# Kernel optimization log

Hardware: AMD Instinct MI355X
Metric: run time of the kernel (lower is better)

The kernel has to match this reference:

```python
import jax, jax.numpy as jnp
import numpy as np


def setup_inputs() -> dict:
    key = jax.random.key(0)
    k1, k2 = jax.random.split(key)
    H, D, N = 1, 256, 65536        # (heads=1, embedding_dim, num_tokens)
    C = 1024                       # num_embeddings (codebook size)
    inputs = jax.random.normal(k1, (H, D, N), dtype=jnp.float32)
    embedding = jax.random.normal(k2, (H, C, D), dtype=jnp.float32)
    return {"inputs": inputs, "embedding": embedding}


COMMITMENT_COST = 0.25


def reference(inputs, embedding):
    # inputs: (h, d, n) -> flat: (h, n, d)
    flat = jnp.transpose(inputs, (0, 2, 1))
    # negative euclidean distance (matches -torch.cdist, p=2)
    x2 = jnp.sum(flat * flat, axis=-1, keepdims=True)            # (h, n, 1)
    e2 = jnp.sum(embedding * embedding, axis=-1)[:, None, :]     # (h, 1, c)
    xe = jnp.einsum('hnd,hcd->hnc', flat, embedding)             # (h, n, c)
    d2 = jnp.maximum(x2 + e2 - 2.0 * xe, 0.0)
    distances = -jnp.sqrt(d2)                                    # (h, n, c)
    encoding_indices = jnp.argmax(distances, axis=2)             # (h, n)
    # gather codebook vectors: h == 1
    quantized = jnp.take(embedding[0], encoding_indices[0], axis=0)[None]  # (h, n, d)
    commit_loss = jnp.mean((jax.lax.stop_gradient(quantized) - flat) ** 2)
    loss = COMMITMENT_COST * commit_loss
    # straight-through estimator
    quantized_st = flat + jax.lax.stop_gradient(quantized - flat)
    out = jnp.transpose(quantized_st, (0, 2, 1))                 # (h, d, n)
    return out, encoding_indices, loss, distances
```

## Files before the change

### kernel.cpp

```cpp
#include <hip/hip_runtime.h>
#include <math.h>

#define N_TOK 65536
#define D_DIM 256
#define C_NUM 1024

#define OUT_OFF   0
#define IDX_OFF   (D_DIM * N_TOK)
#define LOSS_OFF  (IDX_OFF + N_TOK)
#define DIST_OFF  (LOSS_OFF + 1)

#define MARGIN 0.01f
#define NPART 4096

typedef __attribute__((ext_vector_type(8))) short bf16x8;
typedef __attribute__((ext_vector_type(4))) float f32x4;

static __device__ __forceinline__ unsigned short f2bf(float f) {
  unsigned int u = __float_as_uint(f);
  unsigned int r = (u + 0x7fffu + ((u >> 16) & 1u)) >> 16;
  return (unsigned short)r;
}
static __device__ __forceinline__ float bf2f(unsigned short h) {
  return __uint_as_float(((unsigned int)h) << 16);
}


#define WS_EH   0
#define WS_EL   524288
#define WS_E2   1048576
#define WS_NEEDED (WS_E2 + 4096)

#define XH_OFF_F 0
#define XL_OFF_F 8388608

#define PART_OFF_F 263168

__global__ __launch_bounds__(256) void kA2_prep(const float* __restrict__ X,
                                                const float* __restrict__ E,
                                                float* __restrict__ out,
                                                unsigned char* __restrict__ ws) {
  const int bid = blockIdx.x, tid = threadIdx.x;
  if (bid < 1024) {
    unsigned short* XhG = (unsigned short*)(out + XH_OFF_F);
    unsigned short* XlG = (unsigned short*)(out + XL_OFF_F);
    const int n = bid * 64 + (tid >> 2);
    const int sg = (tid & 3) * 16;
    unsigned short* xh = XhG + (size_t)n * D_DIM;
    unsigned short* xl = XlG + (size_t)n * D_DIM;
#pragma unroll 1
    for (int dc = 0; dc < D_DIM; dc += 64) {
      float v[16];
#pragma unroll
      for (int j = 0; j < 16; ++j) v[j] = X[(size_t)(dc + sg + j) * N_TOK + n];
      unsigned short hh[16], ll[16];
#pragma unroll
      for (int j = 0; j < 16; ++j) {
        hh[j] = f2bf(v[j]);
        ll[j] = f2bf(v[j] - bf2f(hh[j]));
      }
      *(bf16x8*)(xh + dc + sg) = *(bf16x8*)&hh[0];
      *(bf16x8*)(xh + dc + sg + 8) = *(bf16x8*)&hh[8];
      *(bf16x8*)(xl + dc + sg) = *(bf16x8*)&ll[0];
      *(bf16x8*)(xl + dc + sg + 8) = *(bf16x8*)&ll[8];
    }
  } else if (bid < 1040) {
    unsigned short* EhG = (unsigned short*)(ws + WS_EH);
    unsigned short* ElG = (unsigned short*)(ws + WS_EL);
    float* e2p = (float*)(ws + WS_E2);
    const int lane = tid & 63, w = tid >> 6;
#pragma unroll 1
    for (int cc = 0; cc < 16; ++cc) {
      const int c = (bid - 1024) * 64 + w * 16 + cc;
      const float4 v = *(const float4*)(E + (size_t)c * D_DIM + lane * 4);
      unsigned short h0 = f2bf(v.x), h1 = f2bf(v.y), h2 = f2bf(v.z), h3 = f2bf(v.w);
      unsigned short l0 = f2bf(v.x - bf2f(h0)), l1 = f2bf(v.y - bf2f(h1));
      unsigned short l2 = f2bf(v.z - bf2f(h2)), l3 = f2bf(v.w - bf2f(h3));
      ushort4 hv = make_ushort4(h0, h1, h2, h3);
      ushort4 lv = make_ushort4(l0, l1, l2, l3);
      *(ushort4*)(EhG + (size_t)c * D_DIM + lane * 4) = hv;
      *(ushort4*)(ElG + (size_t)c * D_DIM + lane * 4) = lv;
      float s = v.x * v.x + v.y * v.y + v.z * v.z + v.w * v.w;
#pragma unroll
      for (int off = 32; off; off >>= 1) s += __shfl_down(s, off, 64);
      if (lane == 0) e2p[c] = s;
    }
  } else {
    const int n = (bid - 1040) * 256 + tid;
    float s = 0.0f;
#pragma unroll 8
    for (int d = 0; d < D_DIM; ++d) {
      float v = X[(size_t)d * N_TOK + n];
      s = fmaf(v, v, s);
    }
    out[IDX_OFF + n] = s;
  }
}

#define TM 64
#define TC 256
#define BK 32
#define XS2 264

__global__ __launch_bounds__(256) void k2c_dist(float* __restrict__ out,
                                                unsigned char* __restrict__ ws) {
  __shared__ __align__(16) unsigned short xh[TM * XS2];
  __shared__ __align__(16) unsigned short xl[TM * XS2];

  const unsigned short* __restrict__ XhG = (const unsigned short*)(out + XH_OFF_F);
  const unsigned short* __restrict__ XlG = (const unsigned short*)(out + XL_OFF_F);
  const unsigned short* __restrict__ EhG = (const unsigned short*)(ws + WS_EH);
  const float* __restrict__ e2p = (const float*)(ws + WS_E2);

  const int tid = threadIdx.x;
  const int lane = tid & 63, wave = tid >> 6;

  const int bid = blockIdx.x;
  const int xcd = bid & 7;
  const int slot = bid >> 3;
  const int bx = slot & 3;
  const int by = xcd * 128 + (slot >> 2);
  const int c0 = bx * TC;
  const int n0 = by * TM;

  const int wc = c0 + wave * 64;
  const int m = lane & 15;
  const int q = lane >> 4;

  {
    const int tl = tid >> 2;
    const int seg = (tid & 3) * 64;
    const unsigned short* gh = XhG + (size_t)(n0 + tl) * D_DIM + seg;
    const unsigned short* gl = XlG + (size_t)(n0 + tl) * D_DIM + seg;
    unsigned short* sh = xh + tl * XS2 + seg;
    unsigned short* sl = xl + tl * XS2 + seg;
#pragma unroll
    for (int j = 0; j < 8; ++j) {
      *(bf16x8*)(sh + j * 8) = *(const bf16x8*)(gh + j * 8);
      *(bf16x8*)(sl + j * 8) = *(const bf16x8*)(gl + j * 8);
    }
  }
  __syncthreads();

  f32x4 acc[4][4];
#pragma unroll
  for (int i = 0; i < 4; ++i)
#pragma unroll
    for (int t = 0; t < 4; ++t) acc[i][t] = (f32x4){0.f, 0.f, 0.f, 0.f};

  const unsigned short* bp[4];
#pragma unroll
  for (int t = 0; t < 4; ++t) bp[t] = EhG + (size_t)(wc + t * 16 + m) * D_DIM + q * 8;
  const size_t loEu = (size_t)(WS_EL - WS_EH) / 2;

#pragma unroll 2
  for (int kb = 0; kb < D_DIM; kb += BK) {
    bf16x8 ah[4], al[4], bh[4], bl[4];
#pragma unroll
    for (int t = 0; t < 4; ++t) {
      bh[t] = *(const bf16x8*)(bp[t] + kb);
      bl[t] = *(const bf16x8*)(bp[t] + loEu + kb);
    }
#pragma unroll
    for (int i = 0; i < 4; ++i) {
      const int ro = (i * 16 + m) * XS2 + kb + q * 8;
      ah[i] = *(const bf16x8*)&xh[ro];
      al[i] = *(const bf16x8*)&xl[ro];
    }
#pragma unroll
    for (int i = 0; i < 4; ++i)
#pragma unroll
      for (int t = 0; t < 4; ++t) {
        acc[i][t] = __builtin_amdgcn_mfma_f32_16x16x32_bf16(ah[i], bh[t], acc[i][t], 0, 0, 0);
        acc[i][t] = __builtin_amdgcn_mfma_f32_16x16x32_bf16(ah[i], bl[t], acc[i][t], 0, 0, 0);
        acc[i][t] = __builtin_amdgcn_mfma_f32_16x16x32_bf16(al[i], bh[t], acc[i][t], 0, 0, 0);
      }
  }

  float e2v[4];
#pragma unroll
  for (int t = 0; t < 4; ++t) e2v[t] = e2p[wc + t * 16 + m];

#pragma unroll
  for (int i = 0; i < 4; ++i) {
#pragma unroll
    for (int r = 0; r < 4; ++r) {
      const int tok = n0 + i * 16 + q * 4 + r;
      const float x2v = out[IDX_OFF + tok];
      const size_t row = DIST_OFF + (size_t)tok * C_NUM;
#pragma unroll
      for (int t = 0; t < 4; ++t) {
        float d2 = fmaf(-2.0f, acc[i][t][r], x2v + e2v[t]);
        d2 = fmaxf(d2, 0.0f);
        out[row + wc + t * 16 + m] = -sqrtf(d2);
      }
    }
  }
}

__global__ __launch_bounds__(256) void k3_argmax(const float* __restrict__ X,
                                                 const float* __restrict__ E,
                                                 float* __restrict__ out) {
  __shared__ float lsum[4];
  const int tid = threadIdx.x, lane = tid & 63, w = tid >> 6;
  float wloss = 0.0f;

#pragma unroll 1
  for (int it = 0; it < 4; ++it) {
    const int n = blockIdx.x * 16 + w * 4 + it;
    const float* row = out + DIST_OFF + (size_t)n * C_NUM;

    float v[16];
    float best = -3.4e38f;
    int bi = 0x7fffffff;
#pragma unroll
    for (int j = 0; j < 16; ++j) {
      v[j] = row[j * 64 + lane];
      if (v[j] > best) { best = v[j]; bi = j * 64 + lane; }
    }
#pragma unroll
    for (int off = 32; off; off >>= 1) {
      const float ov = __shfl_xor(best, off, 64);
      const int oi = __shfl_xor(bi, off, 64);
      if (ov > best || (ov == best && oi < bi)) { best = ov; bi = oi; }
    }
    const float thr = best - MARGIN;
    unsigned long long masks[16];
    int total = 0;
#pragma unroll
    for (int j = 0; j < 16; ++j) {
      masks[j] = __ballot(v[j] > thr);
      total += __popcll(masks[j]);
    }
    float best_d2 = best * best;
    int best_idx = bi;
    if (total > 1) {
      best_d2 = 3.4e38f;
      best_idx = 0x7fffffff;
      for (int j = 0; j < 16; ++j) {
        unsigned long long mm = masks[j];
        while (mm) {
          const int l = __ffsll((long long)mm) - 1;
          mm &= mm - 1;
          const int c = j * 64 + l;
          float sx = 0.f, se = 0.f, sxe = 0.f;
#pragma unroll
          for (int r = 0; r < 4; ++r) {
            const int d = r * 64 + lane;
            const float xv = X[(size_t)d * N_TOK + n];
            const float ev = E[(size_t)c * D_DIM + d];
            sx = fmaf(xv, xv, sx);
            se = fmaf(ev, ev, se);
            sxe = fmaf(xv, ev, sxe);
          }
          float d2 = fmaf(-2.f, sxe, sx + se);
#pragma unroll
          for (int off = 32; off; off >>= 1) d2 += __shfl_xor(d2, off, 64);
          d2 = fmaxf(d2, 0.f);
          if (d2 < best_d2 || (d2 == best_d2 && c < best_idx)) {
            best_d2 = d2; best_idx = c;
          }
        }
      }
    }
    if (lane == 0) out[IDX_OFF + n] = (float)best_idx;
    wloss += best_d2;
  }
  if (lane == 0) lsum[w] = wloss;
  __syncthreads();
  if (tid == 0)
    out[PART_OFF_F + blockIdx.x] = lsum[0] + lsum[1] + lsum[2] + lsum[3];
}

__global__ __launch_bounds__(256) void k3b_loss(float* __restrict__ out) {
  __shared__ float red[4];
  const int tid = threadIdx.x, lane = tid & 63, w = tid >> 6;
  float s = 0.0f;
#pragma unroll
  for (int i = 0; i < NPART / 256; ++i) s += out[PART_OFF_F + i * 256 + tid];
#pragma unroll
  for (int off = 32; off; off >>= 1) s += __shfl_down(s, off, 64);
  if (lane == 0) red[w] = s;
  __syncthreads();
  if (tid == 0)
    out[LOSS_OFF] = (red[0] + red[1] + red[2] + red[3]) *
                    (0.25f / ((float)N_TOK * (float)D_DIM));
}

#define EH_OFF_F  0
#define EL_OFF_F  131072
#define E2_OFF_F  262144

__global__ __launch_bounds__(256) void kA_prep(const float* __restrict__ X,
                                               const float* __restrict__ E,
                                               float* __restrict__ out) {
  const int bid = blockIdx.x, tid = threadIdx.x;
  if (bid < 256) {
    const int n = bid * 256 + tid;
    float s = 0.0f;
#pragma unroll 8
    for (int d = 0; d < D_DIM; ++d) {
      float v = X[(size_t)d * N_TOK + n];
      s = fmaf(v, v, s);
    }
    out[IDX_OFF + n] = s;
  } else {
    unsigned short* EhG = (unsigned short*)(out + EH_OFF_F);
    unsigned short* ElG = (unsigned short*)(out + EL_OFF_F);
    const int lane = tid & 63, w = tid >> 6;
#pragma unroll 1
    for (int cc = 0; cc < 16; ++cc) {
      const int c = (bid - 256) * 64 + w * 16 + cc;
      const float4 v = *(const float4*)(E + (size_t)c * D_DIM + lane * 4);
      unsigned short h0 = f2bf(v.x), h1 = f2bf(v.y), h2 = f2bf(v.z), h3 = f2bf(v.w);
      unsigned short l0 = f2bf(v.x - bf2f(h0)), l1 = f2bf(v.y - bf2f(h1));
      unsigned short l2 = f2bf(v.z - bf2f(h2)), l3 = f2bf(v.w - bf2f(h3));
      ushort4 hv = make_ushort4(h0, h1, h2, h3);
      ushort4 lv = make_ushort4(l0, l1, l2, l3);
      *(ushort4*)(EhG + (size_t)c * D_DIM + lane * 4) = hv;
      *(ushort4*)(ElG + (size_t)c * D_DIM + lane * 4) = lv;
      float s = v.x * v.x + v.y * v.y + v.z * v.z + v.w * v.w;
#pragma unroll
      for (int off = 32; off; off >>= 1) s += __shfl_down(s, off, 64);
      if (lane == 0) out[E2_OFF_F + c] = s;
    }
  }
}

#define XS 40

__global__ __launch_bounds__(256) void k2_dist(const float* __restrict__ X,
                                               float* __restrict__ out) {
  __shared__ __align__(16) unsigned short xhb[2][TM * XS];
  __shared__ __align__(16) unsigned short xlb[2][TM * XS];

  const unsigned short* __restrict__ EhG = (const unsigned short*)(out + EH_OFF_F);
  const unsigned short* __restrict__ ElG = (const unsigned short*)(out + EL_OFF_F);

  const int tid = threadIdx.x;
  const int lane = tid & 63, wave = tid >> 6;
  const int bid = blockIdx.x;
  const int xcd = bid & 7;
  const int slot = bid >> 3;
  const int bx = slot & 3;
  const int by = xcd * 128 + (slot >> 2);
  const int c0 = bx * TC;
  const int n0 = by * TM;

  const int wc = c0 + wave * 64;
  const int m = lane & 15;
  const int q = lane >> 4;

  f32x4 acc[4][4];
#pragma unroll
  for (int i = 0; i < 4; ++i)
#pragma unroll
    for (int t = 0; t < 4; ++t) acc[i][t] = (f32x4){0.f, 0.f, 0.f, 0.f};

  const int sn = lane;
  const int kg = wave;

  float xv[8];
  {
    const float* xp = X + (size_t)(kg * 8) * N_TOK + n0 + sn;
#pragma unroll
    for (int j = 0; j < 8; ++j) xv[j] = xp[(size_t)j * N_TOK];
  }

#pragma unroll 1
  for (int kb = 0; kb < D_DIM; kb += BK) {
    const int p = (kb >> 5) & 1;
    bf16x8 bh[4], bl[4];
#pragma unroll
    for (int t = 0; t < 4; ++t) {
      const size_t eoff = (size_t)(wc + t * 16 + m) * D_DIM + kb + q * 8;
      bh[t] = *(const bf16x8*)(EhG + eoff);
      bl[t] = *(const bf16x8*)(ElG + eoff);
    }
    unsigned short hh[8], ll[8];
#pragma unroll
    for (int j = 0; j < 8; ++j) {
      hh[j] = f2bf(xv[j]);
      ll[j] = f2bf(xv[j] - bf2f(hh[j]));
    }
    *(bf16x8*)&xhb[p][sn * XS + kg * 8] = *(bf16x8*)hh;
    *(bf16x8*)&xlb[p][sn * XS + kg * 8] = *(bf16x8*)ll;
    if (kb + BK < D_DIM) {
      const float* xp = X + (size_t)(kb + BK + kg * 8) * N_TOK + n0 + sn;
#pragma unroll
      for (int j = 0; j < 8; ++j) xv[j] = xp[(size_t)j * N_TOK];
    }
    __syncthreads();
    bf16x8 ah[4], al[4];
#pragma unroll
    for (int i = 0; i < 4; ++i) {
      const int ro = (i * 16 + m) * XS + q * 8;
      ah[i] = *(const bf16x8*)&xhb[p][ro];
      al[i] = *(const bf16x8*)&xlb[p][ro];
    }
#pragma unroll
    for (int i = 0; i < 4; ++i)
#pragma unroll
      for (int t = 0; t < 4; ++t) {
        acc[i][t] = __builtin_amdgcn_mfma_f32_16x16x32_bf16(ah[i], bh[t], acc[i][t], 0, 0, 0);
        acc[i][t] = __builtin_amdgcn_mfma_f32_16x16x32_bf16(ah[i], bl[t], acc[i][t], 0, 0, 0);
        acc[i][t] = __builtin_amdgcn_mfma_f32_16x16x32_bf16(al[i], bh[t], acc[i][t], 0, 0, 0);
      }
  }

  float e2v[4];
#pragma unroll
  for (int t = 0; t < 4; ++t) e2v[t] = out[E2_OFF_F + wc + t * 16 + m];

#pragma unroll
  for (int i = 0; i < 4; ++i) {
#pragma unroll
    for (int r = 0; r < 4; ++r) {
      const int tok = n0 + i * 16 + q * 4 + r;
      const float x2v = out[IDX_OFF + tok];
      const size_t row = DIST_OFF + (size_t)tok * C_NUM;
#pragma unroll
      for (int t = 0; t < 4; ++t) {
        float d2 = fmaf(-2.0f, acc[i][t][r], x2v + e2v[t]);
        d2 = fmaxf(d2, 0.0f);
        out[row + wc + t * 16 + m] = -sqrtf(d2);
      }
    }
  }
}

__global__ __launch_bounds__(256) void k4_gather(const float* __restrict__ E,
                                                 float* __restrict__ out) {
  const int g = blockIdx.x * 256 + threadIdx.x;
  const int n = g * 4;
  const int i0 = (int)out[IDX_OFF + n + 0];
  const int i1 = (int)out[IDX_OFF + n + 1];
  const int i2 = (int)out[IDX_OFF + n + 2];
  const int i3 = (int)out[IDX_OFF + n + 3];
  const float* e0 = E + (size_t)i0 * D_DIM;
  const float* e1 = E + (size_t)i1 * D_DIM;
  const float* e2 = E + (size_t)i2 * D_DIM;
  const float* e3 = E + (size_t)i3 * D_DIM;
  const int d0 = blockIdx.y * 32;
#pragma unroll 4
  for (int d = d0; d < d0 + 32; ++d) {
    float4 wv = make_float4(e0[d], e1[d], e2[d], e3[d]);
    *(float4*)&out[(size_t)d * N_TOK + n] = wv;
  }
}

extern "C" void kernel_launch(void* const* d_in, const int* in_sizes, int n_in,
                              void* d_out, int out_size, void* d_ws, size_t ws_size,
                              hipStream_t stream) {
  const float* X = (const float*)d_in[0];
  const float* E = (const float*)d_in[1];
  float* out = (float*)d_out;

  if (ws_size >= WS_NEEDED && d_ws != nullptr) {
    unsigned char* ws = (unsigned char*)d_ws;
    hipLaunchKernelGGL(kA2_prep, dim3(1296), dim3(256), 0, stream, X, E, out, ws);
    hipLaunchKernelGGL(k2c_dist, dim3((C_NUM / TC) * (N_TOK / TM)), dim3(256), 0,
                       stream, out, ws);
    hipLaunchKernelGGL(k3_argmax, dim3(N_TOK / 16), dim3(256), 0, stream, X, E, out);
    hipLaunchKernelGGL(k3b_loss, dim3(1), dim3(256), 0, stream, out);
    hipLaunchKernelGGL(k4_gather, dim3(N_TOK / 4 / 256, 8), dim3(256), 0, stream,
                       E, out);
  } else {
    hipLaunchKernelGGL(kA_prep, dim3(272), dim3(256), 0, stream, X, E, out);
    hipLaunchKernelGGL(k2_dist, dim3((C_NUM / TC) * (N_TOK / TM)), dim3(256), 0,
                       stream, X, out);
    hipLaunchKernelGGL(k3_argmax, dim3(N_TOK / 16), dim3(256), 0, stream, X, E, out);
    hipLaunchKernelGGL(k3b_loss, dim3(1), dim3(256), 0, stream, out);
    hipLaunchKernelGGL(k4_gather, dim3(N_TOK / 4 / 256, 8), dim3(256), 0, stream,
                       E, out);
  }
}
```

Before: 656.9 us.

## Fuse per-tile argmax partials into distance kernel and software-prefetch B fragments

The distance kernel now computes a per-token, per-64-column best value, index and near-tie count, and writes these to a workspace table. The argmax kernel combines the 16 partials per token and rereads the full 1024-wide distance row only when near-ties need exact fp32 refinement. This is meant to avoid reading the 256 MB distance matrix back in the common case. The K loop of the distance kernel also double-buffers its codebook fragment loads from global memory. In exchange, the epilogue gains shuffles and extra workspace writes, and the workspace requirement grows.

```diff
diff --git a/kernel.cpp b/kernel.cpp
--- a/kernel.cpp
+++ b/kernel.cpp
@@ -29,7 +29,9 @@
 #define WS_EH   0
 #define WS_EL   524288
 #define WS_E2   1048576
-#define WS_NEEDED (WS_E2 + 4096)
+#define WS_PART 1052672
+#define WS_TP   1069056
+#define WS_NEEDED (WS_TP + (size_t)N_TOK * 16 * 8)
 
 #define XH_OFF_F 0
 #define XL_OFF_F 8388608
@@ -111,6 +113,7 @@
   const unsigned short* __restrict__ XlG = (const unsigned short*)(out + XL_OFF_F);
   const unsigned short* __restrict__ EhG = (const unsigned short*)(ws + WS_EH);
   const float* __restrict__ e2p = (const float*)(ws + WS_E2);
+  uint2* __restrict__ tp = (uint2*)(ws + WS_TP);
 
   const int tid = threadIdx.x;
   const int lane = tid & 63, wave = tid >> 6;
@@ -153,14 +156,23 @@
   for (int t = 0; t < 4; ++t) bp[t] = EhG + (size_t)(wc + t * 16 + m) * D_DIM + q * 8;
   const size_t loEu = (size_t)(WS_EL - WS_EH) / 2;
 
-#pragma unroll 2
-  for (int kb = 0; kb < D_DIM; kb += BK) {
-    bf16x8 ah[4], al[4], bh[4], bl[4];
-#pragma unroll
-    for (int t = 0; t < 4; ++t) {
-      bh[t] = *(const bf16x8*)(bp[t] + kb);
-      bl[t] = *(const bf16x8*)(bp[t] + loEu + kb);
-    }
+  bf16x8 bh[4], bl[4], nbh[4], nbl[4];
+#pragma unroll
+  for (int t = 0; t < 4; ++t) {
+    bh[t] = *(const bf16x8*)(bp[t]);
+    bl[t] = *(const bf16x8*)(bp[t] + loEu);
+  }
+#pragma unroll
+  for (int kc = 0; kc < 8; ++kc) {
+    const int kb = kc * BK;
+    if (kc < 7) {
+#pragma unroll
+      for (int t = 0; t < 4; ++t) {
+        nbh[t] = *(const bf16x8*)(bp[t] + kb + BK);
+        nbl[t] = *(const bf16x8*)(bp[t] + loEu + kb + BK);
+      }
+    }
+    bf16x8 ah[4], al[4];
 #pragma unroll
     for (int i = 0; i < 4; ++i) {
       const int ro = (i * 16 + m) * XS2 + kb + q * 8;
@@ -175,6 +187,10 @@
         acc[i][t] = __builtin_amdgcn_mfma_f32_16x16x32_bf16(ah[i], bl[t], acc[i][t], 0, 0, 0);
         acc[i][t] = __builtin_amdgcn_mfma_f32_16x16x32_bf16(al[i], bh[t], acc[i][t], 0, 0, 0);
       }
+    if (kc < 7) {
+#pragma unroll
+      for (int t = 0; t < 4; ++t) { bh[t] = nbh[t]; bl[t] = nbl[t]; }
+    }
   }
 
   float e2v[4];
@@ -188,96 +204,160 @@
       const int tok = n0 + i * 16 + q * 4 + r;
       const float x2v = out[IDX_OFF + tok];
       const size_t row = DIST_OFF + (size_t)tok * C_NUM;
+      float dv[4];
+      float bestv = -3.4e38f;
+      int bidx = 0;
 #pragma unroll
       for (int t = 0; t < 4; ++t) {
         float d2 = fmaf(-2.0f, acc[i][t][r], x2v + e2v[t]);
         d2 = fmaxf(d2, 0.0f);
-        out[row + wc + t * 16 + m] = -sqrtf(d2);
-      }
-    }
-  }
-}
-
-__global__ __launch_bounds__(256) void k3_argmax(const float* __restrict__ X,
-                                                 const float* __restrict__ E,
-                                                 float* __restrict__ out) {
+        const float dd = -sqrtf(d2);
+        dv[t] = dd;
+        out[row + wc + t * 16 + m] = dd;
+        if (dd > bestv) { bestv = dd; bidx = wc + t * 16 + m; }
+      }
+#pragma unroll
+      for (int off = 1; off < 16; off <<= 1) {
+        const float ov = __shfl_xor(bestv, off, 64);
+        const int oi = __shfl_xor(bidx, off, 64);
+        if (ov > bestv || (ov == bestv && oi < bidx)) { bestv = ov; bidx = oi; }
+      }
+      const float thr2 = bestv - MARGIN;
+      int cnt = 0;
+#pragma unroll
+      for (int t = 0; t < 4; ++t) cnt += (dv[t] > thr2) ? 1 : 0;
+#pragma unroll
+      for (int off = 1; off < 16; off <<= 1) cnt += __shfl_xor(cnt, off, 64);
+      if ((lane & 15) == 0) {
+        tp[(size_t)tok * 16 + bx * 4 + wave] =
+            make_uint2(__float_as_uint(bestv),
+                       (unsigned)bidx | ((unsigned)cnt << 16));
+      }
+    }
+  }
+}
+
+__global__ __launch_bounds__(256) void k3a2_argmax(const float* __restrict__ X,
+                                                   const float* __restrict__ E,
+                                                   float* __restrict__ out,
+                                                   unsigned char* __restrict__ ws) {
+  const uint2* __restrict__ tp = (const uint2*)(ws + WS_TP);
+  float* __restrict__ part = (float*)(ws + WS_PART);
   __shared__ float lsum[4];
   const int tid = threadIdx.x, lane = tid & 63, w = tid >> 6;
-  float wloss = 0.0f;
-
-#pragma unroll 1
-  for (int it = 0; it < 4; ++it) {
-    const int n = blockIdx.x * 16 + w * 4 + it;
-    const float* row = out + DIST_OFF + (size_t)n * C_NUM;
-
-    float v[16];
-    float best = -3.4e38f;
-    int bi = 0x7fffffff;
-#pragma unroll
-    for (int j = 0; j < 16; ++j) {
-      v[j] = row[j * 64 + lane];
-      if (v[j] > best) { best = v[j]; bi = j * 64 + lane; }
-    }
-#pragma unroll
-    for (int off = 32; off; off >>= 1) {
-      const float ov = __shfl_xor(best, off, 64);
-      const int oi = __shfl_xor(bi, off, 64);
-      if (ov > best || (ov == best && oi < bi)) { best = ov; bi = oi; }
-    }
-    const float thr = best - MARGIN;
-    unsigned long long masks[16];
-    int total = 0;
-#pragma unroll
-    for (int j = 0; j < 16; ++j) {
-      masks[j] = __ballot(v[j] > thr);
-      total += __popcll(masks[j]);
-    }
-    float best_d2 = best * best;
-    int best_idx = bi;
-    if (total > 1) {
-      best_d2 = 3.4e38f;
-      best_idx = 0x7fffffff;
+  const int g = lane & 15, seg = lane >> 4;
+  const int n = blockIdx.x * 16 + w * 4 + seg;
+
+  const uint2 rec = tp[(size_t)n * 16 + g];
+  const float val = __uint_as_float(rec.x);
+  const int idx = (int)(rec.y & 0xffffu);
+  const int cnt = (int)(rec.y >> 16);
+
+  float best = val;
+  int bi = idx, bc = cnt;
+#pragma unroll
+  for (int off = 1; off < 16; off <<= 1) {
+    const float ov = __shfl_xor(best, off, 64);
+    const int oi = __shfl_xor(bi, off, 64);
+    const int oc = __shfl_xor(bc, off, 64);
+    if (ov > best || (ov == best && oi < bi)) { best = ov; bi = oi; bc = oc; }
+  }
+  const float thr = best - MARGIN;
+  const unsigned long long bal = __ballot(val > thr);
+  const int m16 = (int)((bal >> (seg * 16)) & 0xffffull);
+  const bool fast = (__popc((unsigned)m16) == 1) && (bc == 1);
+
+  float lval = 0.0f;
+  if (fast && g == 0) {
+    out[IDX_OFF + n] = (float)bi;
+    lval = best * best;
+  }
+
+  unsigned long long smask = __ballot((!fast) && (g == 0));
+  float sloss = 0.0f;
+  while (smask) {
+    const int sl = __ffsll((long long)smask) - 1;
+    smask &= smask - 1;
+    const int nn = blockIdx.x * 16 + w * 4 + (sl >> 4);
+    {
+      const float* row = out + DIST_OFF + (size_t)nn * C_NUM;
+      float v[16];
+      float bestf = -3.4e38f;
+      int bif = 0x7fffffff;
+#pragma unroll
       for (int j = 0; j < 16; ++j) {
-        unsigned long long mm = masks[j];
-        while (mm) {
-          const int l = __ffsll((long long)mm) - 1;
-          mm &= mm - 1;
-          const int c = j * 64 + l;
-          float sx = 0.f, se = 0.f, sxe = 0.f;
-#pragma unroll
-          for (int r = 0; r < 4; ++r) {
-            const int d = r * 64 + lane;
-            const float xv = X[(size_t)d * N_TOK + n];
-            const float ev = E[(size_t)c * D_DIM + d];
-            sx = fmaf(xv, xv, sx);
-            se = fmaf(ev, ev, se);
-            sxe = fmaf(xv, ev, sxe);
-          }
-          float d2 = fmaf(-2.f, sxe, sx + se);
-#pragma unroll
-          for (int off = 32; off; off >>= 1) d2 += __shfl_xor(d2, off, 64);
-          d2 = fmaxf(d2, 0.f);
-          if (d2 < best_d2 || (d2 == best_d2 && c < best_idx)) {
-            best_d2 = d2; best_idx = c;
+        v[j] = row[j * 64 + lane];
+        if (v[j] > bestf) { bestf = v[j]; bif = j * 64 + lane; }
+      }
+#pragma unroll
+      for (int off = 32; off; off >>= 1) {
+        const float ov = __shfl_xor(bestf, off, 64);
+        const int oi = __shfl_xor(bif, off, 64);
+        if (ov > bestf || (ov == bestf && oi < bif)) { bestf = ov; bif = oi; }
+      }
+      const float thrf = bestf - MARGIN;
+      unsigned long long masks[16];
+      int total = 0;
+#pragma unroll
+      for (int j = 0; j < 16; ++j) {
+        masks[j] = __ballot(v[j] > thrf);
+        total += __popcll(masks[j]);
+      }
+      float best_d2 = bestf * bestf;
+      int best_idx = bif;
+      if (total > 1) {
+        best_d2 = 3.4e38f;
+        best_idx = 0x7fffffff;
+        for (int j = 0; j < 16; ++j) {
+          unsigned long long mm = masks[j];
+          while (mm) {
+            const int l = __ffsll((long long)mm) - 1;
+            mm &= mm - 1;
+            const int c = j * 64 + l;
+            float sx = 0.f, se = 0.f, sxe = 0.f;
+#pragma unroll
+            for (int r = 0; r < 4; ++r) {
+              const int d = r * 64 + lane;
+              const float xv = X[(size_t)d * N_TOK + nn];
+              const float ev = E[(size_t)c * D_DIM + d];
+              sx = fmaf(xv, xv, sx);
+              se = fmaf(ev, ev, se);
+              sxe = fmaf(xv, ev, sxe);
+            }
+            float d2 = fmaf(-2.f, sxe, sx + se);
+#pragma unroll
+            for (int off = 32; off; off >>= 1) d2 += __shfl_xor(d2, off, 64);
+            d2 = fmaxf(d2, 0.f);
+            if (d2 < best_d2 || (d2 == best_d2 && c < best_idx)) {
+              best_d2 = d2; best_idx = c;
+            }
           }
         }
       }
-    }
-    if (lane == 0) out[IDX_OFF + n] = (float)best_idx;
-    wloss += best_d2;
-  }
-  if (lane == 0) lsum[w] = wloss;
+      if (lane == 0) {
+        out[IDX_OFF + nn] = (float)best_idx;
+        sloss += best_d2;
+      }
+    }
+  }
+
+  float wl = lval + ((lane == 0) ? sloss : 0.0f);
+#pragma unroll
+  for (int off = 32; off; off >>= 1) wl += __shfl_down(wl, off, 64);
+  if (lane == 0) lsum[w] = wl;
   __syncthreads();
   if (tid == 0)
-    out[PART_OFF_F + blockIdx.x] = lsum[0] + lsum[1] + lsum[2] + lsum[3];
-}
-
-__global__ __launch_bounds__(256) void k3b_loss(float* __restrict__ out) {
+    part[blockIdx.x] = lsum[0] + lsum[1] + lsum[2] + lsum[3];
+}
+
+__global__ __launch_bounds__(256) void k3b2_loss(float* __restrict__ out,
+                                                 unsigned char* __restrict__ ws) {
+  const float* __restrict__ part = (const float*)(ws + WS_PART);
   __shared__ float red[4];
   const int tid = threadIdx.x, lane = tid & 63, w = tid >> 6;
   float s = 0.0f;
 #pragma unroll
-  for (int i = 0; i < NPART / 256; ++i) s += out[PART_OFF_F + i * 256 + tid];
+  for (int i = 0; i < NPART / 256; ++i) s += part[i * 256 + tid];
 #pragma unroll
   for (int off = 32; off; off >>= 1) s += __shfl_down(s, off, 64);
   if (lane == 0) red[w] = s;
@@ -429,6 +509,95 @@
   }
 }
 
+__global__ __launch_bounds__(256) void k3_argmax(const float* __restrict__ X,
+                                                 const float* __restrict__ E,
+                                                 float* __restrict__ out) {
+  __shared__ float lsum[4];
+  const int tid = threadIdx.x, lane = tid & 63, w = tid >> 6;
+  float wloss = 0.0f;
+
+#pragma unroll 1
+  for (int it = 0; it < 4; ++it) {
+    const int n = blockIdx.x * 16 + w * 4 + it;
+    const float* row = out + DIST_OFF + (size_t)n * C_NUM;
+
+    float v[16];
+    float best = -3.4e38f;
+    int bi = 0x7fffffff;
+#pragma unroll
+    for (int j = 0; j < 16; ++j) {
+      v[j] = row[j * 64 + lane];
+      if (v[j] > best) { best = v[j]; bi = j * 64 + lane; }
+    }
+#pragma unroll
+    for (int off = 32; off; off >>= 1) {
+      const float ov = __shfl_xor(best, off, 64);
+      const int oi = __shfl_xor(bi, off, 64);
+      if (ov > best || (ov == best && oi < bi)) { best = ov; bi = oi; }
+    }
+    const float thr = best - MARGIN;
+    unsigned long long masks[16];
+    int total = 0;
+#pragma unroll
+    for (int j = 0; j < 16; ++j) {
+      masks[j] = __ballot(v[j] > thr);
+      total += __popcll(masks[j]);
+    }
+    float best_d2 = best * best;
+    int best_idx = bi;
+    if (total > 1) {
+      best_d2 = 3.4e38f;
+      best_idx = 0x7fffffff;
+      for (int j = 0; j < 16; ++j) {
+        unsigned long long mm = masks[j];
+        while (mm) {
+          const int l = __ffsll((long long)mm) - 1;
+          mm &= mm - 1;
+          const int c = j * 64 + l;
+          float sx = 0.f, se = 0.f, sxe = 0.f;
+#pragma unroll
+          for (int r = 0; r < 4; ++r) {
+            const int d = r * 64 + lane;
+            const float xv = X[(size_t)d * N_TOK + n];
+            const float ev = E[(size_t)c * D_DIM + d];
+            sx = fmaf(xv, xv, sx);
+            se = fmaf(ev, ev, se);
+            sxe = fmaf(xv, ev, sxe);
+          }
+          float d2 = fmaf(-2.f, sxe, sx + se);
+#pragma unroll
+          for (int off = 32; off; off >>= 1) d2 += __shfl_xor(d2, off, 64);
+          d2 = fmaxf(d2, 0.f);
+          if (d2 < best_d2 || (d2 == best_d2 && c < best_idx)) {
+            best_d2 = d2; best_idx = c;
+          }
+        }
+      }
+    }
+    if (lane == 0) out[IDX_OFF + n] = (float)best_idx;
+    wloss += best_d2;
+  }
+  if (lane == 0) lsum[w] = wloss;
+  __syncthreads();
+  if (tid == 0)
+    out[PART_OFF_F + blockIdx.x] = lsum[0] + lsum[1] + lsum[2] + lsum[3];
+}
+
+__global__ __launch_bounds__(256) void k3b_loss(float* __restrict__ out) {
+  __shared__ float red[4];
+  const int tid = threadIdx.x, lane = tid & 63, w = tid >> 6;
+  float s = 0.0f;
+#pragma unroll
+  for (int i = 0; i < NPART / 256; ++i) s += out[PART_OFF_F + i * 256 + tid];
+#pragma unroll
+  for (int off = 32; off; off >>= 1) s += __shfl_down(s, off, 64);
+  if (lane == 0) red[w] = s;
+  __syncthreads();
+  if (tid == 0)
+    out[LOSS_OFF] = (red[0] + red[1] + red[2] + red[3]) *
+                    (0.25f / ((float)N_TOK * (float)D_DIM));
+}
+
 __global__ __launch_bounds__(256) void k4_gather(const float* __restrict__ E,
                                                  float* __restrict__ out) {
   const int g = blockIdx.x * 256 + threadIdx.x;
@@ -461,8 +630,9 @@
     hipLaunchKernelGGL(kA2_prep, dim3(1296), dim3(256), 0, stream, X, E, out, ws);
     hipLaunchKernelGGL(k2c_dist, dim3((C_NUM / TC) * (N_TOK / TM)), dim3(256), 0,
                        stream, out, ws);
-    hipLaunchKernelGGL(k3_argmax, dim3(N_TOK / 16), dim3(256), 0, stream, X, E, out);
-    hipLaunchKernelGGL(k3b_loss, dim3(1), dim3(256), 0, stream, out);
+    hipLaunchKernelGGL(k3a2_argmax, dim3(N_TOK / 16), dim3(256), 0, stream,
+                       X, E, out, ws);
+    hipLaunchKernelGGL(k3b2_loss, dim3(1), dim3(256), 0, stream, out, ws);
     hipLaunchKernelGGL(k4_gather, dim3(N_TOK / 4 / 256, 8), dim3(256), 0, stream,
                        E, out);
   } else {
```

New measurement: 658.6 us. No clear change (+0.3%).

## Emit per-chunk row maxima from distance kernel to prune argmax reads

Applied to the files above, without the earlier changes.

The distance kernel now also writes the max distance of each 64-column chunk per token into a workspace buffer. The argmax kernel uses these 16 maxima to find the threshold and reads only the chunks that could hold candidates, instead of rereading the whole 1024-wide distance row. Loss partials move to the workspace. This adds shuffle reductions and extra stores in the GEMM epilogue, and it requires a larger workspace.

```diff
diff --git a/kernel.cpp b/kernel.cpp
--- a/kernel.cpp
+++ b/kernel.cpp
@@ -29,7 +29,9 @@
 #define WS_EH   0
 #define WS_EL   524288
 #define WS_E2   1048576
-#define WS_NEEDED (WS_E2 + 4096)
+#define WS_PART 1052672
+#define WS_TP   1069056
+#define WS_NEEDED (WS_TP + (size_t)N_TOK * 16 * 4)
 
 #define XH_OFF_F 0
 #define XL_OFF_F 8388608
@@ -111,6 +113,7 @@
   const unsigned short* __restrict__ XlG = (const unsigned short*)(out + XL_OFF_F);
   const unsigned short* __restrict__ EhG = (const unsigned short*)(ws + WS_EH);
   const float* __restrict__ e2p = (const float*)(ws + WS_E2);
+  float* __restrict__ tpv = (float*)(ws + WS_TP);
 
   const int tid = threadIdx.x;
   const int lane = tid & 63, wave = tid >> 6;
@@ -188,19 +191,30 @@
       const int tok = n0 + i * 16 + q * 4 + r;
       const float x2v = out[IDX_OFF + tok];
       const size_t row = DIST_OFF + (size_t)tok * C_NUM;
+      float bestv = -3.4e38f;
 #pragma unroll
       for (int t = 0; t < 4; ++t) {
         float d2 = fmaf(-2.0f, acc[i][t][r], x2v + e2v[t]);
         d2 = fmaxf(d2, 0.0f);
-        out[row + wc + t * 16 + m] = -sqrtf(d2);
-      }
-    }
-  }
-}
-
-__global__ __launch_bounds__(256) void k3_argmax(const float* __restrict__ X,
-                                                 const float* __restrict__ E,
-                                                 float* __restrict__ out) {
+        const float dd = -sqrtf(d2);
+        out[row + wc + t * 16 + m] = dd;
+        bestv = fmaxf(bestv, dd);
+      }
+#pragma unroll
+      for (int off = 1; off < 16; off <<= 1)
+        bestv = fmaxf(bestv, __shfl_xor(bestv, off, 64));
+      if ((lane & 15) == 0)
+        tpv[(size_t)tok * 16 + bx * 4 + wave] = bestv;
+    }
+  }
+}
+
+__global__ __launch_bounds__(256) void k3a3_argmax(const float* __restrict__ X,
+                                                   const float* __restrict__ E,
+                                                   float* __restrict__ out,
+                                                   unsigned char* __restrict__ ws) {
+  const float* __restrict__ tpv = (const float*)(ws + WS_TP);
+  float* __restrict__ part = (float*)(ws + WS_PART);
   __shared__ float lsum[4];
   const int tid = threadIdx.x, lane = tid & 63, w = tid >> 6;
   float wloss = 0.0f;
@@ -210,35 +224,46 @@
     const int n = blockIdx.x * 16 + w * 4 + it;
     const float* row = out + DIST_OFF + (size_t)n * C_NUM;
 
-    float v[16];
-    float best = -3.4e38f;
+    const float gval = tpv[(size_t)n * 16 + (lane & 15)];
+    float best = gval;
+#pragma unroll
+    for (int off = 1; off < 16; off <<= 1)
+      best = fmaxf(best, __shfl_xor(best, off, 64));
+    const float thr = best - MARGIN;
+    const unsigned fmask = (unsigned)(__ballot(gval > thr) & 0xffffull);
+
+    float bestv = -3.4e38f;
     int bi = 0x7fffffff;
-#pragma unroll
-    for (int j = 0; j < 16; ++j) {
-      v[j] = row[j * 64 + lane];
-      if (v[j] > best) { best = v[j]; bi = j * 64 + lane; }
-    }
-#pragma unroll
-    for (int off = 32; off; off >>= 1) {
-      const float ov = __shfl_xor(best, off, 64);
-      const int oi = __shfl_xor(bi, off, 64);
-      if (ov > best || (ov == best && oi < bi)) { best = ov; bi = oi; }
-    }
-    const float thr = best - MARGIN;
-    unsigned long long masks[16];
     int total = 0;
-#pragma unroll
-    for (int j = 0; j < 16; ++j) {
-      masks[j] = __ballot(v[j] > thr);
-      total += __popcll(masks[j]);
-    }
-    float best_d2 = best * best;
-    int best_idx = bi;
-    if (total > 1) {
-      best_d2 = 3.4e38f;
-      best_idx = 0x7fffffff;
-      for (int j = 0; j < 16; ++j) {
-        unsigned long long mm = masks[j];
+    unsigned fm = fmask;
+    while (fm) {
+      const int j = __ffs(fm) - 1;
+      fm &= fm - 1;
+      const float v = row[j * 64 + lane];
+      float bv = v;
+      int bix = j * 64 + lane;
+#pragma unroll
+      for (int off = 32; off; off >>= 1) {
+        const float ov = __shfl_xor(bv, off, 64);
+        const int oi = __shfl_xor(bix, off, 64);
+        if (ov > bv || (ov == bv && oi < bix)) { bv = ov; bix = oi; }
+      }
+      if (bv > bestv || (bv == bestv && bix < bi)) { bestv = bv; bi = bix; }
+      total += __popcll(__ballot(v > thr));
+    }
+
+    if (total == 1) {
+      if (lane == 0) out[IDX_OFF + n] = (float)bi;
+      wloss += bestv * bestv;
+    } else {
+      float best_d2 = 3.4e38f;
+      int best_idx = 0x7fffffff;
+      unsigned fm2 = fmask;
+      while (fm2) {
+        const int j = __ffs(fm2) - 1;
+        fm2 &= fm2 - 1;
+        const float v = row[j * 64 + lane];
+        unsigned long long mm = __ballot(v > thr);
         while (mm) {
           const int l = __ffsll((long long)mm) - 1;
           mm &= mm - 1;
@@ -262,22 +287,24 @@
           }
         }
       }
-    }
-    if (lane == 0) out[IDX_OFF + n] = (float)best_idx;
-    wloss += best_d2;
+      if (lane == 0) out[IDX_OFF + n] = (float)best_idx;
+      wloss += best_d2;
+    }
   }
   if (lane == 0) lsum[w] = wloss;
   __syncthreads();
   if (tid == 0)
-    out[PART_OFF_F + blockIdx.x] = lsum[0] + lsum[1] + lsum[2] + lsum[3];
-}
-
-__global__ __launch_bounds__(256) void k3b_loss(float* __restrict__ out) {
+    part[blockIdx.x] = lsum[0] + lsum[1] + lsum[2] + lsum[3];
+}
+
+__global__ __launch_bounds__(256) void k3b2_loss(float* __restrict__ out,
+                                                 unsigned char* __restrict__ ws) {
+  const float* __restrict__ part = (const float*)(ws + WS_PART);
   __shared__ float red[4];
   const int tid = threadIdx.x, lane = tid & 63, w = tid >> 6;
   float s = 0.0f;
 #pragma unroll
-  for (int i = 0; i < NPART / 256; ++i) s += out[PART_OFF_F + i * 256 + tid];
+  for (int i = 0; i < NPART / 256; ++i) s += part[i * 256 + tid];
 #pragma unroll
   for (int off = 32; off; off >>= 1) s += __shfl_down(s, off, 64);
   if (lane == 0) red[w] = s;
@@ -429,6 +456,95 @@
   }
 }
 
+__global__ __launch_bounds__(256) void k3_argmax(const float* __restrict__ X,
+                                                 const float* __restrict__ E,
+                                                 float* __restrict__ out) {
+  __shared__ float lsum[4];
+  const int tid = threadIdx.x, lane = tid & 63, w = tid >> 6;
+  float wloss = 0.0f;
+
+#pragma unroll 1
+  for (int it = 0; it < 4; ++it) {
+    const int n = blockIdx.x * 16 + w * 4 + it;
+    const float* row = out + DIST_OFF + (size_t)n * C_NUM;
+
+    float v[16];
+    float best = -3.4e38f;
+    int bi = 0x7fffffff;
+#pragma unroll
+    for (int j = 0; j < 16; ++j) {
+      v[j] = row[j * 64 + lane];
+      if (v[j] > best) { best = v[j]; bi = j * 64 + lane; }
+    }
+#pragma unroll
+    for (int off = 32; off; off >>= 1) {
+      const float ov = __shfl_xor(best, off, 64);
+      const int oi = __shfl_xor(bi, off, 64);
+      if (ov > best || (ov == best && oi < bi)) { best = ov; bi = oi; }
+    }
+    const float thr = best - MARGIN;
+    unsigned long long masks[16];
+    int total = 0;
+#pragma unroll
+    for (int j = 0; j < 16; ++j) {
+      masks[j] = __ballot(v[j] > thr);
+      total += __popcll(masks[j]);
+    }
+    float best_d2 = best * best;
+    int best_idx = bi;
+    if (total > 1) {
+      best_d2 = 3.4e38f;
+      best_idx = 0x7fffffff;
+      for (int j = 0; j < 16; ++j) {
+        unsigned long long mm = masks[j];
+        while (mm) {
+          const int l = __ffsll((long long)mm) - 1;
+          mm &= mm - 1;
+          const int c = j * 64 + l;
+          float sx = 0.f, se = 0.f, sxe = 0.f;
+#pragma unroll
+          for (int r = 0; r < 4; ++r) {
+            const int d = r * 64 + lane;
+            const float xv = X[(size_t)d * N_TOK + n];
+            const float ev = E[(size_t)c * D_DIM + d];
+            sx = fmaf(xv, xv, sx);
+            se = fmaf(ev, ev, se);
+            sxe = fmaf(xv, ev, sxe);
+          }
+          float d2 = fmaf(-2.f, sxe, sx + se);
+#pragma unroll
+          for (int off = 32; off; off >>= 1) d2 += __shfl_xor(d2, off, 64);
+          d2 = fmaxf(d2, 0.f);
+          if (d2 < best_d2 || (d2 == best_d2 && c < best_idx)) {
+            best_d2 = d2; best_idx = c;
+          }
+        }
+      }
+    }
+    if (lane == 0) out[IDX_OFF + n] = (float)best_idx;
+    wloss += best_d2;
+  }
+  if (lane == 0) lsum[w] = wloss;
+  __syncthreads();
+  if (tid == 0)
+    out[PART_OFF_F + blockIdx.x] = lsum[0] + lsum[1] + lsum[2] + lsum[3];
+}
+
+__global__ __launch_bounds__(256) void k3b_loss(float* __restrict__ out) {
+  __shared__ float red[4];
+  const int tid = threadIdx.x, lane = tid & 63, w = tid >> 6;
+  float s = 0.0f;
+#pragma unroll
+  for (int i = 0; i < NPART / 256; ++i) s += out[PART_OFF_F + i * 256 + tid];
+#pragma unroll
+  for (int off = 32; off; off >>= 1) s += __shfl_down(s, off, 64);
+  if (lane == 0) red[w] = s;
+  __syncthreads();
+  if (tid == 0)
+    out[LOSS_OFF] = (red[0] + red[1] + red[2] + red[3]) *
+                    (0.25f / ((float)N_TOK * (float)D_DIM));
+}
+
 __global__ __launch_bounds__(256) void k4_gather(const float* __restrict__ E,
                                                  float* __restrict__ out) {
   const int g = blockIdx.x * 256 + threadIdx.x;
@@ -461,8 +577,9 @@
     hipLaunchKernelGGL(kA2_prep, dim3(1296), dim3(256), 0, stream, X, E, out, ws);
     hipLaunchKernelGGL(k2c_dist, dim3((C_NUM / TC) * (N_TOK / TM)), dim3(256), 0,
                        stream, out, ws);
-    hipLaunchKernelGGL(k3_argmax, dim3(N_TOK / 16), dim3(256), 0, stream, X, E, out);
-    hipLaunchKernelGGL(k3b_loss, dim3(1), dim3(256), 0, stream, out);
+    hipLaunchKernelGGL(k3a3_argmax, dim3(N_TOK / 16), dim3(256), 0, stream,
+                       X, E, out, ws);
+    hipLaunchKernelGGL(k3b2_loss, dim3(1), dim3(256), 0, stream, out, ws);
     hipLaunchKernelGGL(k4_gather, dim3(N_TOK / 4 / 256, 8), dim3(256), 0, stream,
                        E, out);
   } else {
```

Result: faster. 641.7 us (-2.3%).
